# Optimization experiments

Measured on AMD Instinct MI355X. Metric: run time of the kernel, lower is better.

## Reference

```python
import jax, jax.numpy as jnp
import numpy as np

HIDDEN = 768
NUM_HEADS = 12
HEAD_SIZE = HIDDEN // NUM_HEADS
LN_EPS = 1e-5


def setup_inputs() -> dict:
    key = jax.random.key(0)
    ks = jax.random.split(key, 10)
    B, S, H = 2, 4096, HIDDEN
    std = 1.0 / np.sqrt(H)
    inp = {
        "hidden_states": jax.random.normal(ks[0], (B, S, H), dtype=jnp.float32),
        "attention_mask": jnp.ones((B, S), dtype=jnp.float32),
        "Wq": jax.random.normal(ks[1], (H, H), dtype=jnp.float32) * std,
        "bq": jnp.zeros((H,), dtype=jnp.float32),
        "Wk": jax.random.normal(ks[2], (H, H), dtype=jnp.float32) * std,
        "bk": jnp.zeros((H,), dtype=jnp.float32),
        "Wv": jax.random.normal(ks[3], (H, H), dtype=jnp.float32) * std,
        "bv": jnp.zeros((H,), dtype=jnp.float32),
        "Wo": jax.random.normal(ks[4], (H, H), dtype=jnp.float32) * std,
        "bo": jnp.zeros((H,), dtype=jnp.float32),
        "ln_gamma": jnp.ones((H,), dtype=jnp.float32),
        "ln_beta": jnp.zeros((H,), dtype=jnp.float32),
    }
    return inp


def _split_heads(x):
    # [B, S, H] -> [B, nH, S, hd]
    B, S, _ = x.shape
    return x.reshape(B, S, NUM_HEADS, HEAD_SIZE).transpose(0, 2, 1, 3)


def reference(hidden_states, attention_mask, Wq, bq, Wk, bk, Wv, bv, Wo, bo, ln_gamma, ln_beta):
    # QKV projections (torch Linear: x @ W.T + b; here W is stored as [in, out])
    q = _split_heads(hidden_states @ Wq + bq)
    k = _split_heads(hidden_states @ Wk + bk)
    v = _split_heads(hidden_states @ Wv + bv)

    scores = jnp.einsum("bhqd,bhkd->bhqk", q, k) / jnp.sqrt(jnp.float32(HEAD_SIZE))
    # additive mask: (1 - mask) * -10000, broadcast over heads and query positions
    scores = scores + (1.0 - attention_mask)[:, None, None, :] * -10000.0
    probs = jax.nn.softmax(scores, axis=-1)  # dropout_prob = 0 -> identity

    ctx = jnp.einsum("bhqk,bhkd->bhqd", probs, v)
    B, _, S, _ = ctx.shape
    ctx = ctx.transpose(0, 2, 1, 3).reshape(B, S, HIDDEN)

    out = ctx @ Wo + bo
    resid = out + hidden_states
    mu = jnp.mean(resid, axis=-1, keepdims=True)
    var = jnp.var(resid, axis=-1, keepdims=True)
    return (resid - mu) * jax.lax.rsqrt(var + LN_EPS) * ln_gamma + ln_beta
```

## Files before the change

kernel.cpp:

```cpp
#include <hip/hip_runtime.h>
#include <hip/hip_bf16.h>

#define HID 768
#define NHEADS 12
#define HDIM 64
#define SEQ 4096
#define BB 2
#define MTOT (BB * SEQ)

typedef __attribute__((ext_vector_type(8))) short bf16x8;
typedef __attribute__((ext_vector_type(16))) float f32x16;

__device__ inline unsigned pack2bf(float a, float b) {
    __hip_bfloat162 h = __float22bfloat162_rn(float2{a, b});
    return *(unsigned*)&h;
}

__global__ __launch_bounds__(256) void cast_x_kernel(
    const float* __restrict__ X, __hip_bfloat16* __restrict__ Xb)
{
    const size_t i = ((size_t)blockIdx.x * 256 + threadIdx.x) * 8;
    const float4 x0 = *(const float4*)(X + i);
    const float4 x1 = *(const float4*)(X + i + 4);
    unsigned u[4];
    u[0] = pack2bf(x0.x, x0.y);
    u[1] = pack2bf(x0.z, x0.w);
    u[2] = pack2bf(x1.x, x1.y);
    u[3] = pack2bf(x1.z, x1.w);
    *(uint4*)(Xb + i) = *(uint4*)u;
}

__global__ __launch_bounds__(256) void pack_w_kernel(
    const float* __restrict__ Wq, const float* __restrict__ Wk,
    const float* __restrict__ Wv, const float* __restrict__ Wo,
    __hip_bfloat16* __restrict__ Wt)
{
    const int z = blockIdx.z;
    const float* __restrict__ W = (z == 0) ? Wq : (z == 1) ? Wk : (z == 2) ? Wv : Wo;
    const int in0  = blockIdx.x * 64;
    const int out0 = blockIdx.y * 64;
    const int t = threadIdx.x;

    __shared__ float T[64][65];
#pragma unroll
    for (int i = 0; i < 4; ++i) {
        const int idx = t + 256 * i;
        const int row = idx >> 4;
        const int c4  = (idx & 15) << 2;
        const float4 v = *(const float4*)(W + (size_t)(in0 + row) * HID + out0 + c4);
        T[row][c4 + 0] = v.x; T[row][c4 + 1] = v.y;
        T[row][c4 + 2] = v.z; T[row][c4 + 3] = v.w;
    }
    __syncthreads();

    const int o  = t >> 2;
    const int cb = (t & 3) << 4;
    __hip_bfloat16 tmp[16];
#pragma unroll
    for (int k = 0; k < 16; ++k)
        tmp[k] = __float2bfloat16(T[cb + k][o]);
    __hip_bfloat16* __restrict__ dst =
        Wt + (size_t)(z * HID + out0 + o) * HID + in0 + cb;
    *(uint4*)(dst)     = *(uint4*)(&tmp[0]);
    *(uint4*)(dst + 8) = *(uint4*)(&tmp[8]);
}

__global__ __launch_bounds__(256) void qkv_mfma_kernel(
    const __hip_bfloat16* __restrict__ Xb, const __hip_bfloat16* __restrict__ Wt,
    const float* __restrict__ bq, const float* __restrict__ bk,
    const float* __restrict__ bv,
    __hip_bfloat16* __restrict__ Qo, __hip_bfloat16* __restrict__ Ko,
    __hip_bfloat16* __restrict__ Vo)
{
    const int nblk = blockIdx.x;
    const int z  = nblk / 6;
    const int f0 = (nblk % 6) * 128;
    const int n0 = nblk * 128;
    const int m0 = blockIdx.y * 128;

    const float* __restrict__ bias = (z == 0) ? bq : (z == 1) ? bk : bv;
    __hip_bfloat16* __restrict__ Out = (z == 0) ? Qo : (z == 1) ? Ko : Vo;

    const int t    = threadIdx.x;
    const int w    = t >> 6;
    const int lane = t & 63;
    const int col  = lane & 31;
    const int g    = lane >> 5;
    const int wm   = w & 1;
    const int wn   = w >> 1;

    __shared__ __hip_bfloat16 As[128][72];
    __shared__ __hip_bfloat16 Bs[128][72];

    f32x16 acc[2][2];
#pragma unroll
    for (int mt = 0; mt < 2; ++mt)
#pragma unroll
        for (int nt = 0; nt < 2; ++nt)
#pragma unroll
            for (int r = 0; r < 16; ++r) acc[mt][nt][r] = 0.f;

    for (int k0 = 0; k0 < HID; k0 += 64) {
        __syncthreads();
#pragma unroll
        for (int i = 0; i < 4; ++i) {
            const int idx = t + 256 * i;
            const int row = idx >> 3;
            const int c8  = (idx & 7) << 3;
            *(uint4*)&As[row][c8] = *(const uint4*)(Xb + (size_t)(m0 + row) * HID + k0 + c8);
            *(uint4*)&Bs[row][c8] = *(const uint4*)(Wt + (size_t)(n0 + row) * HID + k0 + c8);
        }
        __syncthreads();
#pragma unroll
        for (int kh = 0; kh < 4; ++kh) {
            const int ko = 16 * kh + 8 * g;
            const bf16x8 a0 = *(const bf16x8*)&As[64 * wm + col][ko];
            const bf16x8 a1 = *(const bf16x8*)&As[64 * wm + 32 + col][ko];
            const bf16x8 b0 = *(const bf16x8*)&Bs[64 * wn + col][ko];
            const bf16x8 b1 = *(const bf16x8*)&Bs[64 * wn + 32 + col][ko];
            acc[0][0] = __builtin_amdgcn_mfma_f32_32x32x16_bf16(a0, b0, acc[0][0], 0, 0, 0);
            acc[0][1] = __builtin_amdgcn_mfma_f32_32x32x16_bf16(a0, b1, acc[0][1], 0, 0, 0);
            acc[1][0] = __builtin_amdgcn_mfma_f32_32x32x16_bf16(a1, b0, acc[1][0], 0, 0, 0);
            acc[1][1] = __builtin_amdgcn_mfma_f32_32x32x16_bf16(a1, b1, acc[1][1], 0, 0, 0);
        }
    }

    const int h = (f0 >> 6) + wn;
#pragma unroll
    for (int mt = 0; mt < 2; ++mt)
#pragma unroll
        for (int nt = 0; nt < 2; ++nt) {
            const int d = 32 * nt + col;
            const float bsv = bias[f0 + 64 * wn + d];
#pragma unroll
            for (int r = 0; r < 16; ++r) {
                const int m = m0 + 64 * wm + 32 * mt + (r & 3) + 8 * (r >> 2) + 4 * g;
                const int b = m >> 12;
                const int s = m & (SEQ - 1);
                Out[(((size_t)(b * NHEADS + h)) * SEQ + s) * HDIM + d] =
                    __float2bfloat16(acc[mt][nt][r] + bsv);
            }
        }
}

__global__ __launch_bounds__(256) void transpose_v_kernel(
    const __hip_bfloat16* __restrict__ Vb, __hip_bfloat16* __restrict__ Vt)
{
    const int s0 = blockIdx.x * 64;
    const int bh = blockIdx.y;
    const int t  = threadIdx.x;

    __shared__ __hip_bfloat16 Ts[64][72];

#pragma unroll
    for (int i = 0; i < 2; ++i) {
        const int idx = t + 256 * i;
        const int row = idx >> 3;
        const int c8  = (idx & 7) << 3;
        *(uint4*)&Ts[row][c8] =
            *(const uint4*)(Vb + ((size_t)bh * SEQ + s0 + row) * HDIM + c8);
    }
    __syncthreads();

    const int d  = t >> 2;
    const int sb = (t & 3) << 4;
    __hip_bfloat16 tmp[16];
#pragma unroll
    for (int k = 0; k < 16; ++k)
        tmp[k] = Ts[sb + k][d];
    __hip_bfloat16* __restrict__ dst = Vt + ((size_t)bh * HDIM + d) * SEQ + s0 + sb;
    *(uint4*)(dst)     = *(uint4*)(&tmp[0]);
    *(uint4*)(dst + 8) = *(uint4*)(&tmp[8]);
}

__global__ __launch_bounds__(256, 2) void attn_kernel(
    const __hip_bfloat16* __restrict__ Qb, const __hip_bfloat16* __restrict__ Kb,
    const __hip_bfloat16* __restrict__ Vt, const float* __restrict__ mask,
    __hip_bfloat16* __restrict__ Op, float* __restrict__ lp)
{
    const int bh = blockIdx.y;
    const int b  = bh / NHEADS;
    const int h  = bh - b * NHEADS;
    const int kspan = SEQ / gridDim.z;
    const int kbeg  = blockIdx.z * kspan;

    const int t    = threadIdx.x;
    const int w    = t >> 6;
    const int lane = t & 63;
    const int col  = lane & 31;
    const int g    = lane >> 5;
    const int qw   = blockIdx.x * 256 + 64 * w;

    __shared__ __hip_bfloat16 Ks[64][72];
    __shared__ __hip_bfloat16 Vts[64][72];
    __shared__ float madd[64];

    const __hip_bfloat16* __restrict__ Qh = Qb + (size_t)bh * SEQ * HDIM;
    const __hip_bfloat16* __restrict__ Kh = Kb + (size_t)bh * SEQ * HDIM;
    const __hip_bfloat16* __restrict__ Vh = Vt + (size_t)bh * HDIM * SEQ;

    bf16x8 bq[2][4];
#pragma unroll
    for (int mt = 0; mt < 2; ++mt)
#pragma unroll
        for (int kh = 0; kh < 4; ++kh)
            bq[mt][kh] = *(const bf16x8*)(Qh + (size_t)(qw + 32 * mt + col) * HDIM
                                          + 16 * kh + 8 * g);

    f32x16 O[2][2];
    float lac[2] = {0.f, 0.f};
#pragma unroll
    for (int mt = 0; mt < 2; ++mt)
#pragma unroll
        for (int dt = 0; dt < 2; ++dt)
#pragma unroll
            for (int r = 0; r < 16; ++r) O[mt][dt][r] = 0.f;

    for (int kt0 = 0; kt0 < kspan; kt0 += 64) {
        const int kt = kbeg + kt0;
        __syncthreads();
#pragma unroll
        for (int i = 0; i < 2; ++i) {
            const int idx = t + 256 * i;
            const int row = idx >> 3;
            const int c8  = (idx & 7) << 3;
            *(uint4*)&Ks[row][c8]  = *(const uint4*)(Kh + (size_t)(kt + row) * HDIM + c8);
            *(uint4*)&Vts[row][c8] = *(const uint4*)(Vh + (size_t)row * SEQ + kt + c8);
        }
        if (t < 64) madd[t] = (1.0f - mask[b * SEQ + kt + t]) * -10000.0f;
        __syncthreads();

        f32x16 St[2][2];
#pragma unroll
        for (int mt = 0; mt < 2; ++mt)
#pragma unroll
            for (int nt = 0; nt < 2; ++nt)
#pragma unroll
                for (int r = 0; r < 16; ++r) St[mt][nt][r] = 0.f;

#pragma unroll
        for (int kh = 0; kh < 4; ++kh) {
            const bf16x8 ak0 = *(const bf16x8*)&Ks[col][16 * kh + 8 * g];
            const bf16x8 ak1 = *(const bf16x8*)&Ks[32 + col][16 * kh + 8 * g];
            St[0][0] = __builtin_amdgcn_mfma_f32_32x32x16_bf16(ak0, bq[0][kh], St[0][0], 0, 0, 0);
            St[1][0] = __builtin_amdgcn_mfma_f32_32x32x16_bf16(ak0, bq[1][kh], St[1][0], 0, 0, 0);
            St[0][1] = __builtin_amdgcn_mfma_f32_32x32x16_bf16(ak1, bq[0][kh], St[0][1], 0, 0, 0);
            St[1][1] = __builtin_amdgcn_mfma_f32_32x32x16_bf16(ak1, bq[1][kh], St[1][1], 0, 0, 0);
        }

#pragma unroll
        for (int mt = 0; mt < 2; ++mt) {
            unsigned g4x[2][4], g4y[2][4];
#pragma unroll
            for (int nt = 0; nt < 2; ++nt) {
#pragma unroll
                for (int b4 = 0; b4 < 4; ++b4) {
                    const float4 mm = *(const float4*)&madd[32 * nt + 8 * b4 + 4 * g];
                    const float p0 = __expf(fminf(fmaf(St[mt][nt][4 * b4 + 0], 0.125f, mm.x), 30.f));
                    const float p1 = __expf(fminf(fmaf(St[mt][nt][4 * b4 + 1], 0.125f, mm.y), 30.f));
                    const float p2 = __expf(fminf(fmaf(St[mt][nt][4 * b4 + 2], 0.125f, mm.z), 30.f));
                    const float p3 = __expf(fminf(fmaf(St[mt][nt][4 * b4 + 3], 0.125f, mm.w), 30.f));
                    lac[mt] += (p0 + p1) + (p2 + p3);
                    g4x[nt][b4] = pack2bf(p0, p1);
                    g4y[nt][b4] = pack2bf(p2, p3);
                }
            }
#pragma unroll
            for (int kh = 0; kh < 4; ++kh) {
                const int nt  = kh >> 1;
                const int khl = kh & 1;
                const unsigned lo_x = g4x[nt][2 * khl],     lo_y = g4y[nt][2 * khl];
                const unsigned hi_x = g4x[nt][2 * khl + 1], hi_y = g4y[nt][2 * khl + 1];
                const unsigned sx = g ? lo_x : hi_x;
                const unsigned sy = g ? lo_y : hi_y;
                const unsigned rx = (unsigned)__shfl_xor((int)sx, 32, 64);
                const unsigned ry = (unsigned)__shfl_xor((int)sy, 32, 64);
                union { unsigned u[4]; bf16x8 v; } au;
                if (g) { au.u[0] = rx; au.u[1] = ry; au.u[2] = hi_x; au.u[3] = hi_y; }
                else   { au.u[0] = lo_x; au.u[1] = lo_y; au.u[2] = rx; au.u[3] = ry; }
                const bf16x8 bv0 = *(const bf16x8*)&Vts[col][16 * kh + 8 * g];
                const bf16x8 bv1 = *(const bf16x8*)&Vts[32 + col][16 * kh + 8 * g];
                O[mt][0] = __builtin_amdgcn_mfma_f32_32x32x16_bf16(au.v, bv0, O[mt][0], 0, 0, 0);
                O[mt][1] = __builtin_amdgcn_mfma_f32_32x32x16_bf16(au.v, bv1, O[mt][1], 0, 0, 0);
            }
        }
    }

    const size_t opbase = (size_t)blockIdx.z * ((size_t)MTOT * HID);
#pragma unroll
    for (int mt = 0; mt < 2; ++mt) {
        const float l = lac[mt] + __shfl_xor(lac[mt], 32, 64);
        if (g == 0)
            lp[((size_t)blockIdx.z * (BB * NHEADS) + bh) * SEQ + qw + 32 * mt + col] = l;
#pragma unroll
        for (int dt = 0; dt < 2; ++dt)
#pragma unroll
            for (int r = 0; r < 16; ++r) {
                const int q = qw + 32 * mt + (r & 3) + 8 * (r >> 2) + 4 * g;
                const int d = 32 * dt + col;
                Op[opbase + ((size_t)b * SEQ + q) * HID + h * HDIM + d] =
                    __float2bfloat16(O[mt][dt][r]);
            }
    }
}

__global__ __launch_bounds__(256) void combine_kernel(
    const __hip_bfloat16* __restrict__ Op, const float* __restrict__ lp,
    __hip_bfloat16* __restrict__ Ctx, int KS)
{
    const size_t i = ((size_t)blockIdx.x * 256 + threadIdx.x) * 8;
    const int n   = (int)(i % HID);
    const int row = (int)(i / HID);
    const int h = n >> 6;
    const int b = row >> 12;
    const int q = row & (SEQ - 1);
    const int bh = b * NHEADS + h;

    float denom = 0.f;
    float o[8] = {};
    for (int kz = 0; kz < KS; ++kz) {
        denom += lp[((size_t)kz * (BB * NHEADS) + bh) * SEQ + q];
        uint4 u = *(const uint4*)(Op + (size_t)kz * ((size_t)MTOT * HID) + i);
        const __hip_bfloat16* e = (const __hip_bfloat16*)&u;
#pragma unroll
        for (int j = 0; j < 8; ++j) o[j] += __bfloat162float(e[j]);
    }
    const float inv = 1.0f / denom;
    unsigned u[4];
#pragma unroll
    for (int j = 0; j < 4; ++j)
        u[j] = pack2bf(o[2 * j] * inv, o[2 * j + 1] * inv);
    *(uint4*)(Ctx + i) = *(uint4*)u;
}

__global__ __launch_bounds__(256) void out_mfma_kernel(
    const __hip_bfloat16* __restrict__ Cb, const __hip_bfloat16* __restrict__ Wto,
    const float* __restrict__ bo, const float* __restrict__ X,
    float* __restrict__ Resid)
{
    const int n0 = blockIdx.x * 128;
    const int m0 = blockIdx.y * 128;

    const int t    = threadIdx.x;
    const int w    = t >> 6;
    const int lane = t & 63;
    const int col  = lane & 31;
    const int g    = lane >> 5;
    const int wm   = w & 1;
    const int wn   = w >> 1;

    __shared__ __hip_bfloat16 As[128][72];
    __shared__ __hip_bfloat16 Bs[128][72];

    f32x16 acc[2][2];
#pragma unroll
    for (int mt = 0; mt < 2; ++mt)
#pragma unroll
        for (int nt = 0; nt < 2; ++nt)
#pragma unroll
            for (int r = 0; r < 16; ++r) acc[mt][nt][r] = 0.f;

    for (int k0 = 0; k0 < HID; k0 += 64) {
        __syncthreads();
#pragma unroll
        for (int i = 0; i < 4; ++i) {
            const int idx = t + 256 * i;
            const int row = idx >> 3;
            const int c8  = (idx & 7) << 3;
            *(uint4*)&As[row][c8] = *(const uint4*)(Cb  + (size_t)(m0 + row) * HID + k0 + c8);
            *(uint4*)&Bs[row][c8] = *(const uint4*)(Wto + (size_t)(n0 + row) * HID + k0 + c8);
        }
        __syncthreads();
#pragma unroll
        for (int kh = 0; kh < 4; ++kh) {
            const int ko = 16 * kh + 8 * g;
            const bf16x8 a0 = *(const bf16x8*)&As[64 * wm + col][ko];
            const bf16x8 a1 = *(const bf16x8*)&As[64 * wm + 32 + col][ko];
            const bf16x8 b0 = *(const bf16x8*)&Bs[64 * wn + col][ko];
            const bf16x8 b1 = *(const bf16x8*)&Bs[64 * wn + 32 + col][ko];
            acc[0][0] = __builtin_amdgcn_mfma_f32_32x32x16_bf16(a0, b0, acc[0][0], 0, 0, 0);
            acc[0][1] = __builtin_amdgcn_mfma_f32_32x32x16_bf16(a0, b1, acc[0][1], 0, 0, 0);
            acc[1][0] = __builtin_amdgcn_mfma_f32_32x32x16_bf16(a1, b0, acc[1][0], 0, 0, 0);
            acc[1][1] = __builtin_amdgcn_mfma_f32_32x32x16_bf16(a1, b1, acc[1][1], 0, 0, 0);
        }
    }

#pragma unroll
    for (int mt = 0; mt < 2; ++mt)
#pragma unroll
        for (int nt = 0; nt < 2; ++nt) {
            const int n = n0 + 64 * wn + 32 * nt + col;
            const float bsv = bo[n];
#pragma unroll
            for (int r = 0; r < 16; ++r) {
                const int m = m0 + 64 * wm + 32 * mt + (r & 3) + 8 * (r >> 2) + 4 * g;
                Resid[(size_t)m * HID + n] = acc[mt][nt][r] + bsv + X[(size_t)m * HID + n];
            }
        }
}

__global__ __launch_bounds__(256) void ln_kernel(
    const float* __restrict__ Rin, const float* __restrict__ gamma,
    const float* __restrict__ beta, float* __restrict__ Out)
{
    const int row = blockIdx.x;
    const int t   = threadIdx.x;
    const float* __restrict__ x = Rin + (size_t)row * HID;

    const float v0 = x[t];
    const float v1 = x[t + 256];
    const float v2 = x[t + 512];
    float s  = v0 + v1 + v2;
    float s2 = v0 * v0 + v1 * v1 + v2 * v2;
#pragma unroll
    for (int off = 32; off; off >>= 1) {
        s  += __shfl_xor(s,  off, 64);
        s2 += __shfl_xor(s2, off, 64);
    }
    __shared__ float rs[4], rs2[4];
    const int w = t >> 6, lane = t & 63;
    if (lane == 0) { rs[w] = s; rs2[w] = s2; }
    __syncthreads();
    const float tot  = rs[0] + rs[1] + rs[2] + rs[3];
    const float tot2 = rs2[0] + rs2[1] + rs2[2] + rs2[3];
    const float mu   = tot * (1.0f / HID);
    const float var  = tot2 * (1.0f / HID) - mu * mu;
    const float rsig = rsqrtf(var + 1e-5f);

    float* __restrict__ y = Out + (size_t)row * HID;
    y[t]       = (v0 - mu) * rsig * gamma[t]       + beta[t];
    y[t + 256] = (v1 - mu) * rsig * gamma[t + 256] + beta[t + 256];
    y[t + 512] = (v2 - mu) * rsig * gamma[t + 512] + beta[t + 512];
}

extern "C" void kernel_launch(void* const* d_in, const int* in_sizes, int n_in,
                              void* d_out, int out_size, void* d_ws, size_t ws_size,
                              hipStream_t stream)
{
    const float* X     = (const float*)d_in[0];
    const float* mask  = (const float*)d_in[1];
    const float* Wq    = (const float*)d_in[2];
    const float* bq    = (const float*)d_in[3];
    const float* Wk    = (const float*)d_in[4];
    const float* bk    = (const float*)d_in[5];
    const float* Wv    = (const float*)d_in[6];
    const float* bv    = (const float*)d_in[7];
    const float* Wo    = (const float*)d_in[8];
    const float* bo    = (const float*)d_in[9];
    const float* gamma = (const float*)d_in[10];
    const float* beta  = (const float*)d_in[11];
    float* out = (float*)d_out;

    const size_t N = (size_t)MTOT * HID;
    const size_t WTE = (size_t)4 * HID * HID;

    char* p = (char*)d_ws;
    __hip_bfloat16* Xb  = (__hip_bfloat16*)p;  p += 2 * N;
    __hip_bfloat16* Wt  = (__hip_bfloat16*)p;  p += 2 * WTE;
    __hip_bfloat16* Qw  = (__hip_bfloat16*)p;  p += 2 * N;
    __hip_bfloat16* Kw  = (__hip_bfloat16*)p;  p += 2 * N;
    __hip_bfloat16* Vw  = (__hip_bfloat16*)p;  p += 2 * N;
    __hip_bfloat16* Vtw = (__hip_bfloat16*)p;  p += 2 * N;
    char* opb = p;
    const size_t fixed = (size_t)(opb - (char*)d_ws);

    const size_t lpsz4 = 4 * (size_t)(BB * NHEADS) * SEQ * sizeof(float);
    const int KS = (ws_size >= fixed + 4 * 2 * N + lpsz4) ? 4 : 2;

    __hip_bfloat16* Op  = (__hip_bfloat16*)opb;
    float* lpt = (float*)(opb + (size_t)KS * 2 * N);
    float* Rd  = (float*)opb;
    __hip_bfloat16* Ctxb = Vw;

    cast_x_kernel<<<(int)(N / 2048), 256, 0, stream>>>(X, Xb);
    pack_w_kernel<<<dim3(12, 12, 4), 256, 0, stream>>>(Wq, Wk, Wv, Wo, Wt);
    qkv_mfma_kernel<<<dim3(18, MTOT / 128), 256, 0, stream>>>(
        Xb, Wt, bq, bk, bv, Qw, Kw, Vw);
    transpose_v_kernel<<<dim3(SEQ / 64, BB * NHEADS), 256, 0, stream>>>(Vw, Vtw);
    attn_kernel<<<dim3(SEQ / 256, BB * NHEADS, KS), 256, 0, stream>>>(
        Qw, Kw, Vtw, mask, Op, lpt);
    combine_kernel<<<(int)(N / 2048), 256, 0, stream>>>(Op, lpt, Ctxb, KS);
    out_mfma_kernel<<<dim3(6, MTOT / 128), 256, 0, stream>>>(
        Ctxb, Wt + (size_t)2304 * HID, bo, X, Rd);
    ln_kernel<<<MTOT, 256, 0, stream>>>(Rd, gamma, beta, out);
}
```

Before: 352.2 us.

## Fuse split-K attention combine into output projection and use exp2 softmax

Removes the separate combine kernel. The output-projection GEMM now sums the KS partial attention outputs, divides by the summed softmax denominators (precomputed per tile in shared memory), and packs the result into its A tile on load. This drops one full write and re-read of the context tensor. The cost is that each of the 6 N-column blocks redoes the partial reads and reductions, and the residual buffer moves to the K workspace. Separately, softmax now uses a hardware exp2 with the log2(e) factor folded into the scale and the mask, and the clamp at 30 is removed, which risks overflow for large scores.

Measured after the change: 403.1 us. 14.4% more time.

```diff
diff --git a/kernel.cpp b/kernel.cpp
--- a/kernel.cpp
+++ b/kernel.cpp
@@ -10,6 +10,8 @@
 
 typedef __attribute__((ext_vector_type(8))) short bf16x8;
 typedef __attribute__((ext_vector_type(16))) float f32x16;
+
+#define LOG2E 1.4426950408889634f
 
 __device__ inline unsigned pack2bf(float a, float b) {
     __hip_bfloat162 h = __float22bfloat162_rn(float2{a, b});
@@ -216,6 +218,8 @@
 #pragma unroll
             for (int r = 0; r < 16; ++r) O[mt][dt][r] = 0.f;
 
+    const float kscale = 0.125f * LOG2E;
+
     for (int kt0 = 0; kt0 < kspan; kt0 += 64) {
         const int kt = kbeg + kt0;
         __syncthreads();
@@ -227,7 +231,7 @@
             *(uint4*)&Ks[row][c8]  = *(const uint4*)(Kh + (size_t)(kt + row) * HDIM + c8);
             *(uint4*)&Vts[row][c8] = *(const uint4*)(Vh + (size_t)row * SEQ + kt + c8);
         }
-        if (t < 64) madd[t] = (1.0f - mask[b * SEQ + kt + t]) * -10000.0f;
+        if (t < 64) madd[t] = (1.0f - mask[b * SEQ + kt + t]) * (-10000.0f * LOG2E);
         __syncthreads();
 
         f32x16 St[2][2];
@@ -256,10 +260,10 @@
 #pragma unroll
                 for (int b4 = 0; b4 < 4; ++b4) {
                     const float4 mm = *(const float4*)&madd[32 * nt + 8 * b4 + 4 * g];
-                    const float p0 = __expf(fminf(fmaf(St[mt][nt][4 * b4 + 0], 0.125f, mm.x), 30.f));
-                    const float p1 = __expf(fminf(fmaf(St[mt][nt][4 * b4 + 1], 0.125f, mm.y), 30.f));
-                    const float p2 = __expf(fminf(fmaf(St[mt][nt][4 * b4 + 2], 0.125f, mm.z), 30.f));
-                    const float p3 = __expf(fminf(fmaf(St[mt][nt][4 * b4 + 3], 0.125f, mm.w), 30.f));
+                    const float p0 = __builtin_amdgcn_exp2f(fmaf(St[mt][nt][4 * b4 + 0], kscale, mm.x));
+                    const float p1 = __builtin_amdgcn_exp2f(fmaf(St[mt][nt][4 * b4 + 1], kscale, mm.y));
+                    const float p2 = __builtin_amdgcn_exp2f(fmaf(St[mt][nt][4 * b4 + 2], kscale, mm.z));
+                    const float p3 = __builtin_amdgcn_exp2f(fmaf(St[mt][nt][4 * b4 + 3], kscale, mm.w));
                     lac[mt] += (p0 + p1) + (p2 + p3);
                     g4x[nt][b4] = pack2bf(p0, p1);
                     g4y[nt][b4] = pack2bf(p2, p3);
@@ -304,42 +308,14 @@
     }
 }
 
-__global__ __launch_bounds__(256) void combine_kernel(
+__global__ __launch_bounds__(256) void out_mfma_kernel(
     const __hip_bfloat16* __restrict__ Op, const float* __restrict__ lp,
-    __hip_bfloat16* __restrict__ Ctx, int KS)
-{
-    const size_t i = ((size_t)blockIdx.x * 256 + threadIdx.x) * 8;
-    const int n   = (int)(i % HID);
-    const int row = (int)(i / HID);
-    const int h = n >> 6;
-    const int b = row >> 12;
-    const int q = row & (SEQ - 1);
-    const int bh = b * NHEADS + h;
-
-    float denom = 0.f;
-    float o[8] = {};
-    for (int kz = 0; kz < KS; ++kz) {
-        denom += lp[((size_t)kz * (BB * NHEADS) + bh) * SEQ + q];
-        uint4 u = *(const uint4*)(Op + (size_t)kz * ((size_t)MTOT * HID) + i);
-        const __hip_bfloat16* e = (const __hip_bfloat16*)&u;
-#pragma unroll
-        for (int j = 0; j < 8; ++j) o[j] += __bfloat162float(e[j]);
-    }
-    const float inv = 1.0f / denom;
-    unsigned u[4];
-#pragma unroll
-    for (int j = 0; j < 4; ++j)
-        u[j] = pack2bf(o[2 * j] * inv, o[2 * j + 1] * inv);
-    *(uint4*)(Ctx + i) = *(uint4*)u;
-}
-
-__global__ __launch_bounds__(256) void out_mfma_kernel(
-    const __hip_bfloat16* __restrict__ Cb, const __hip_bfloat16* __restrict__ Wto,
-    const float* __restrict__ bo, const float* __restrict__ X,
-    float* __restrict__ Resid)
+    const __hip_bfloat16* __restrict__ Wto, const float* __restrict__ bo,
+    const float* __restrict__ X, float* __restrict__ Resid, int KS)
 {
     const int n0 = blockIdx.x * 128;
     const int m0 = blockIdx.y * 128;
+    const size_t NN = (size_t)MTOT * HID;
 
     const int t    = threadIdx.x;
     const int w    = t >> 6;
@@ -351,6 +327,20 @@
 
     __shared__ __hip_bfloat16 As[128][72];
     __shared__ __hip_bfloat16 Bs[128][72];
+    __shared__ float linv_s[NHEADS][128];
+
+    for (int i = t; i < NHEADS * 128; i += 256) {
+        const int hh  = i >> 7;
+        const int row = i & 127;
+        const int m   = m0 + row;
+        const int b   = m >> 12;
+        const int q   = m & (SEQ - 1);
+        const int bh  = b * NHEADS + hh;
+        float lsum = 0.f;
+        for (int kz = 0; kz < KS; ++kz)
+            lsum += lp[((size_t)kz * (BB * NHEADS) + bh) * SEQ + q];
+        linv_s[hh][row] = 1.0f / lsum;
+    }
 
     f32x16 acc[2][2];
 #pragma unroll
@@ -361,13 +351,27 @@
             for (int r = 0; r < 16; ++r) acc[mt][nt][r] = 0.f;
 
     for (int k0 = 0; k0 < HID; k0 += 64) {
+        const int hseg = k0 >> 6;
         __syncthreads();
 #pragma unroll
         for (int i = 0; i < 4; ++i) {
             const int idx = t + 256 * i;
             const int row = idx >> 3;
             const int c8  = (idx & 7) << 3;
-            *(uint4*)&As[row][c8] = *(const uint4*)(Cb  + (size_t)(m0 + row) * HID + k0 + c8);
+            float o[8] = {};
+            for (int kz = 0; kz < KS; ++kz) {
+                uint4 u = *(const uint4*)(Op + (size_t)kz * NN
+                                          + (size_t)(m0 + row) * HID + k0 + c8);
+                const __hip_bfloat16* e = (const __hip_bfloat16*)&u;
+#pragma unroll
+                for (int j = 0; j < 8; ++j) o[j] += __bfloat162float(e[j]);
+            }
+            const float inv = linv_s[hseg][row];
+            unsigned pu[4];
+#pragma unroll
+            for (int j = 0; j < 4; ++j)
+                pu[j] = pack2bf(o[2 * j] * inv, o[2 * j + 1] * inv);
+            *(uint4*)&As[row][c8] = *(uint4*)pu;
             *(uint4*)&Bs[row][c8] = *(const uint4*)(Wto + (size_t)(n0 + row) * HID + k0 + c8);
         }
         __syncthreads();
@@ -469,8 +473,7 @@
 
     __hip_bfloat16* Op  = (__hip_bfloat16*)opb;
     float* lpt = (float*)(opb + (size_t)KS * 2 * N);
-    float* Rd  = (float*)opb;
-    __hip_bfloat16* Ctxb = Vw;
+    float* Rd  = (float*)Kw;
 
     cast_x_kernel<<<(int)(N / 2048), 256, 0, stream>>>(X, Xb);
     pack_w_kernel<<<dim3(12, 12, 4), 256, 0, stream>>>(Wq, Wk, Wv, Wo, Wt);
@@ -479,8 +482,7 @@
     transpose_v_kernel<<<dim3(SEQ / 64, BB * NHEADS), 256, 0, stream>>>(Vw, Vtw);
     attn_kernel<<<dim3(SEQ / 256, BB * NHEADS, KS), 256, 0, stream>>>(
         Qw, Kw, Vtw, mask, Op, lpt);
-    combine_kernel<<<(int)(N / 2048), 256, 0, stream>>>(Op, lpt, Ctxb, KS);
     out_mfma_kernel<<<dim3(6, MTOT / 128), 256, 0, stream>>>(
-        Ctxb, Wt + (size_t)2304 * HID, bo, X, Rd);
+        Op, lpt, Wt + (size_t)2304 * HID, bo, X, Rd, KS);
     ln_kernel<<<MTOT, 256, 0, stream>>>(Rd, gamma, beta, out);
 }
```
